# Kernel tuning notes

Hardware: AMD Instinct MI355X
Metric: run time of the kernel (lower is better)

Reference implementation:

```python
import jax, jax.numpy as jnp
import numpy as np

N_NODES = 100000
N_EDGES = 1600000
IN_FEATS = 128
HID = 128
N_GRAPHS = 1024


def setup_inputs() -> dict:
    key = jax.random.key(0)
    ks = jax.random.split(key, 10)
    h = jax.random.normal(ks[0], (N_NODES, IN_FEATS), dtype=jnp.float32)
    src = jax.random.randint(ks[1], (N_EDGES,), 0, N_NODES)
    dst = jax.random.randint(ks[2], (N_EDGES,), 0, N_NODES)
    graph_ids = jnp.sort(jax.random.randint(ks[3], (N_NODES,), 0, N_GRAPHS))
    # parameters (Glorot-ish scale)
    W1 = jax.random.normal(ks[4], (IN_FEATS, HID), dtype=jnp.float32) / np.sqrt(IN_FEATS)
    b1 = jnp.zeros((HID,), dtype=jnp.float32)
    W2 = jax.random.normal(ks[5], (HID, HID), dtype=jnp.float32) / np.sqrt(HID)
    b2 = jnp.zeros((HID,), dtype=jnp.float32)
    fc_w = jax.random.normal(ks[6], (HID, 1), dtype=jnp.float32) / np.sqrt(HID)
    fc_b = jnp.zeros((1,), dtype=jnp.float32)
    return {"h": h, "src": src, "dst": dst, "graph_ids": graph_ids,
            "n_graphs": N_GRAPHS, "W1": W1, "b1": b1, "W2": W2, "b2": b2,
            "fc_w": fc_w, "fc_b": fc_b}


def _graph_conv(x, W, b, src, dst, c_src, c_dst):
    # DGL GraphConv, norm='both': scale by out_deg^-1/2 at src, aggregate, scale by in_deg^-1/2 at dst
    x = (x * c_src) @ W                      # [N, out]
    agg = jax.ops.segment_sum(x[src], dst, num_segments=x.shape[0])  # SpMM via gather+scatter
    return agg * c_dst + b


def reference(h, src, dst, graph_ids, n_graphs, W1, b1, W2, b2, fc_w, fc_b):
    n = h.shape[0]
    ones_e = jnp.ones(src.shape[0], dtype=h.dtype)
    out_deg = jnp.clip(jax.ops.segment_sum(ones_e, src, num_segments=n), 1.0)
    in_deg = jnp.clip(jax.ops.segment_sum(ones_e, dst, num_segments=n), 1.0)
    c_src = (out_deg ** -0.5)[:, None]
    c_dst = (in_deg ** -0.5)[:, None]

    x = jax.nn.relu(_graph_conv(h, W1, b1, src, dst, c_src, c_dst))
    x = jax.nn.relu(_graph_conv(x, W2, b2, src, dst, c_src, c_dst))

    # dgl.mean_nodes: per-graph mean over nodes
    sums = jax.ops.segment_sum(x, graph_ids, num_segments=n_graphs)        # [G, HID]
    cnts = jnp.clip(jax.ops.segment_sum(jnp.ones((n,), x.dtype), graph_ids,
                                        num_segments=n_graphs), 1.0)
    hg = sums / cnts[:, None]
    return (hg @ fc_w + fc_b).squeeze(-1)    # [G]
```

## Files before the change

kernel.cpp:

```cpp
#include <hip/hip_runtime.h>


#define RANGE 256
#define NBMAX 1024
#define EPB 4096
#define CAP 5120

typedef __attribute__((ext_vector_type(4))) float facc4;
typedef __attribute__((ext_vector_type(8))) short bfrag8;

__device__ inline unsigned short f2bf(float x) {
  unsigned u = __float_as_uint(x);
  u += 0x7FFFu + ((u >> 16) & 1u);
  return (unsigned short)(u >> 16);
}
__device__ inline float bf2f(unsigned short b) {
  return __uint_as_float((unsigned)b << 16);
}
__device__ inline float bflo(unsigned u) { return __uint_as_float(u << 16); }
__device__ inline float bfhi(unsigned u) { return __uint_as_float(u & 0xFFFF0000u); }

__device__ inline void acc8(float* a, const uint4 v) {
  a[0] += bflo(v.x); a[1] += bfhi(v.x);
  a[2] += bflo(v.y); a[3] += bfhi(v.y);
  a[4] += bflo(v.z); a[5] += bfhi(v.z);
  a[6] += bflo(v.w); a[7] += bfhi(v.w);
}

__device__ inline void gather_node(const int* __restrict__ esrc,
                                   const unsigned short* __restrict__ Y,
                                   int beg, int end, int fo, float* acc) {
  int e = beg;
  for (; e < end && (e & 3); ++e) {
    const uint4 v = *(const uint4*)(Y + (size_t)esrc[e] * 128 + fo);
    acc8(acc, v);
  }
  for (; e + 8 <= end; e += 8) {
    const int4 s0 = *(const int4*)(esrc + e);
    const int4 s1 = *(const int4*)(esrc + e + 4);
    const uint4 v0 = *(const uint4*)(Y + (size_t)s0.x * 128 + fo);
    const uint4 v1 = *(const uint4*)(Y + (size_t)s0.y * 128 + fo);
    const uint4 v2 = *(const uint4*)(Y + (size_t)s0.z * 128 + fo);
    const uint4 v3 = *(const uint4*)(Y + (size_t)s0.w * 128 + fo);
    const uint4 v4 = *(const uint4*)(Y + (size_t)s1.x * 128 + fo);
    const uint4 v5 = *(const uint4*)(Y + (size_t)s1.y * 128 + fo);
    const uint4 v6 = *(const uint4*)(Y + (size_t)s1.z * 128 + fo);
    const uint4 v7 = *(const uint4*)(Y + (size_t)s1.w * 128 + fo);
    acc8(acc, v0); acc8(acc, v1); acc8(acc, v2); acc8(acc, v3);
    acc8(acc, v4); acc8(acc, v5); acc8(acc, v6); acc8(acc, v7);
  }
  if (e + 4 <= end) {
    const int4 s0 = *(const int4*)(esrc + e);
    const uint4 v0 = *(const uint4*)(Y + (size_t)s0.x * 128 + fo);
    const uint4 v1 = *(const uint4*)(Y + (size_t)s0.y * 128 + fo);
    const uint4 v2 = *(const uint4*)(Y + (size_t)s0.z * 128 + fo);
    const uint4 v3 = *(const uint4*)(Y + (size_t)s0.w * 128 + fo);
    acc8(acc, v0); acc8(acc, v1); acc8(acc, v2); acc8(acc, v3);
    e += 4;
  }
  for (; e < end; ++e) {
    const uint4 v = *(const uint4*)(Y + (size_t)esrc[e] * 128 + fo);
    acc8(acc, v);
  }
}

__global__ __launch_bounds__(256) void k_part(const int* __restrict__ src,
                                              const int* __restrict__ dst,
                                              int* __restrict__ curS,
                                              int* __restrict__ curD,
                                              unsigned char* __restrict__ outS,
                                              unsigned int* __restrict__ outD,
                                              int E, int NB) {
  __shared__ int sS[EPB];
  __shared__ int sD[EPB];
  __shared__ int hS[NBMAX];
  __shared__ int hD[NBMAX];
  const int t = threadIdx.x;
  for (int i = t; i < NB; i += 256) { hS[i] = 0; hD[i] = 0; }
  __syncthreads();
  const int e0 = blockIdx.x * EPB;
  #pragma unroll
  for (int i = 0; i < EPB / 256; ++i) {
    const int e = e0 + t + 256 * i;
    if (e < E) {
      const int sv = src[e], dv = dst[e];
      sS[t + 256 * i] = sv;
      sD[t + 256 * i] = dv;
      atomicAdd(&hS[sv >> 8], 1);
      atomicAdd(&hD[dv >> 8], 1);
    }
  }
  __syncthreads();
  for (int i = t; i < NB; i += 256) {
    int c = hS[i];
    hS[i] = c ? atomicAdd(&curS[i], c) : 0;
    c = hD[i];
    hD[i] = c ? atomicAdd(&curD[i], c) : 0;
  }
  __syncthreads();
  #pragma unroll
  for (int i = 0; i < EPB / 256; ++i) {
    const int e = e0 + t + 256 * i;
    if (e < E) {
      const int sv = sS[t + 256 * i], dv = sD[t + 256 * i];
      int p = atomicAdd(&hS[sv >> 8], 1);
      if (p < CAP) outS[(size_t)(sv >> 8) * CAP + p] = (unsigned char)(sv & 255);
      p = atomicAdd(&hD[dv >> 8], 1);
      if (p < CAP)
        outD[(size_t)(dv >> 8) * CAP + p] =
            ((unsigned)(dv & 255) << 24) | (unsigned)sv;
    }
  }
}

__global__ __launch_bounds__(256) void k_prep(
    const unsigned int* __restrict__ outD, const int* __restrict__ curD,
    int2* __restrict__ rng, int* __restrict__ esrc, float* __restrict__ cD,
    const unsigned char* __restrict__ outS, const int* __restrict__ curS,
    float* __restrict__ cS, const int* __restrict__ gid,
    int* __restrict__ gstart, float* __restrict__ gsum,
    int N, int NB, int G, int nbN) {
  __shared__ int hist[RANGE];
  __shared__ int scn[RANGE];
  const int b = blockIdx.x;
  const int t = threadIdx.x;

  if (b < NB) {
    const int beg = b * CAP;
    const int cnt = min(curD[b], CAP);
    hist[t] = 0;
    __syncthreads();
    for (int e = t; e < cnt; e += 256)
      atomicAdd(&hist[outD[beg + e] >> 24], 1);
    __syncthreads();
    const int deg = hist[t];
    scn[t] = deg;
    __syncthreads();
    #pragma unroll
    for (int o = 1; o < RANGE; o <<= 1) {
      int u = (t >= o) ? scn[t - o] : 0;
      __syncthreads();
      scn[t] += u;
      __syncthreads();
    }
    const int excl = scn[t] - deg;
    const int node = b * RANGE + t;
    if (node < N) {
      cD[node] = rsqrtf((float)(deg > 1 ? deg : 1));
      rng[node] = make_int2(beg + excl, beg + excl + deg);
    }
    scn[t] = excl;
    __syncthreads();
    for (int e = t; e < cnt; e += 256) {
      const unsigned w = outD[beg + e];
      const int pos = beg + atomicAdd(&scn[w >> 24], 1);
      esrc[pos] = (int)(w & 0x1FFFFu);
    }
  } else if (b < 2 * NB) {
    const int bb = b - NB;
    const int beg = bb * CAP;
    const int cnt = min(curS[bb], CAP);
    hist[t] = 0;
    __syncthreads();
    for (int e = t; e < cnt; e += 256)
      atomicAdd(&hist[outS[beg + e]], 1);
    __syncthreads();
    const int node = bb * RANGE + t;
    if (node < N) cS[node] = rsqrtf((float)(hist[t] > 1 ? hist[t] : 1));
  } else if (b < 2 * NB + nbN) {
    const int i = (b - 2 * NB) * 256 + t;
    if (i < N) {
      const int g = gid[i];
      if (i == 0) {
        for (int q = 0; q <= g; ++q) gstart[q] = 0;
      } else {
        const int gp = gid[i - 1];
        for (int q = gp + 1; q <= g; ++q) gstart[q] = i;
      }
      if (i == N - 1) {
        for (int q = g + 1; q <= G; ++q) gstart[q] = N;
      }
    }
  } else {
    const int i = (b - 2 * NB - nbN) * 256 + t;
    if (i < G) gsum[i] = 0.f;
  }
}

__global__ __launch_bounds__(256) void k_wprep2(const float* __restrict__ W1,
                                                const float* __restrict__ W2,
                                                unsigned short* __restrict__ Whi,
                                                unsigned short* __restrict__ Wlo) {
  const int g = blockIdx.x * 256 + threadIdx.x;
  const float* W = (g < 16384) ? W1 : W2;
  const int idx = g & 16383;
  const int i = idx & 7;
  const int l = (idx >> 3) & 63;
  const int nb = (idx >> 9) & 7;
  const int kc = idx >> 12;
  const int k = kc * 32 + ((l >> 4) << 3) + i;
  const int n = (nb << 4) + (l & 15);
  const float v = W[k * 128 + n];
  const unsigned short hi = f2bf(v);
  Whi[g] = hi;
  Wlo[g] = f2bf(v - bf2f(hi));
}

__global__ __launch_bounds__(256) void k_mgemm0(const float* __restrict__ Xf,
                                                const unsigned short* __restrict__ Whi,
                                                const unsigned short* __restrict__ Wlo,
                                                const float* __restrict__ cS,
                                                unsigned short* __restrict__ Y,
                                                int N) {
  const int t = threadIdx.x;
  const int wv = t >> 6;
  const int l = t & 63;
  const int lm = l & 15;
  const int lg = l >> 4;
  const int row0 = (blockIdx.x * 4 + wv) * 16;
  const int row = row0 + lm;
  const bool rv = row < N;
  const int rc = rv ? row : 0;
  const float csr = rv ? cS[rc] : 0.f;

  facc4 acc[8];
  #pragma unroll
  for (int nb = 0; nb < 8; ++nb) acc[nb] = (facc4){0.f, 0.f, 0.f, 0.f};

  #pragma unroll
  for (int kc = 0; kc < 4; ++kc) {
    const int k0 = kc * 32 + (lg << 3);
    const float4 x0 = *(const float4*)(Xf + (size_t)rc * 128 + k0);
    const float4 x1 = *(const float4*)(Xf + (size_t)rc * 128 + k0 + 4);
    float a[8] = {x0.x, x0.y, x0.z, x0.w, x1.x, x1.y, x1.z, x1.w};
    #pragma unroll
    for (int i = 0; i < 8; ++i) a[i] *= csr;
    bfrag8 ah, al;
    #pragma unroll
    for (int i = 0; i < 8; ++i) {
      const unsigned short hh = f2bf(a[i]);
      ah[i] = (short)hh;
      al[i] = (short)f2bf(a[i] - bf2f(hh));
    }
    const size_t kb = ((size_t)kc * 8) * 512 + (size_t)l * 8;
    #pragma unroll
    for (int nb = 0; nb < 8; ++nb) {
      const bfrag8 bh = *(const bfrag8*)(Whi + kb + (size_t)nb * 512);
      const bfrag8 bl = *(const bfrag8*)(Wlo + kb + (size_t)nb * 512);
      acc[nb] = __builtin_amdgcn_mfma_f32_16x16x32_bf16(ah, bh, acc[nb], 0, 0, 0);
      acc[nb] = __builtin_amdgcn_mfma_f32_16x16x32_bf16(ah, bl, acc[nb], 0, 0, 0);
      acc[nb] = __builtin_amdgcn_mfma_f32_16x16x32_bf16(al, bh, acc[nb], 0, 0, 0);
    }
  }

  #pragma unroll
  for (int j = 0; j < 4; ++j) {
    const int r = row0 + (lg << 2) + j;
    if (r < N) {
      #pragma unroll
      for (int nb = 0; nb < 8; ++nb)
        Y[(size_t)r * 128 + (nb << 4) + lm] = f2bf(acc[nb][j]);
    }
  }
}

__global__ __launch_bounds__(256) void k_gspmm(
    const int2* __restrict__ rng, const int* __restrict__ esrc,
    const unsigned short* __restrict__ Y1,
    const unsigned short* __restrict__ Whi,
    const unsigned short* __restrict__ Wlo,
    const float* __restrict__ cS, const float* __restrict__ cD,
    const float* __restrict__ bias, unsigned short* __restrict__ Y2, int N) {
  __shared__ float As[64][132];
  const int t = threadIdx.x;
  const int base = blockIdx.x * 64;

  {
    const int lane = t & 15;
    const int grp = t >> 4;
    const int fo = lane * 8;
    #pragma unroll
    for (int s = 0; s < 4; ++s) {
      const int nl = s * 16 + grp;
      const int node = base + nl;
      float acc[8] = {0.f, 0.f, 0.f, 0.f, 0.f, 0.f, 0.f, 0.f};
      if (node < N) {
        const int2 be = rng[node];
        gather_node(esrc, Y1, be.x, be.y, fo, acc);
      }
      *(float4*)&As[nl][fo] = make_float4(acc[0], acc[1], acc[2], acc[3]);
      *(float4*)&As[nl][fo + 4] = make_float4(acc[4], acc[5], acc[6], acc[7]);
    }
  }
  __syncthreads();

  const int wv = t >> 6;
  const int l = t & 63;
  const int lm = l & 15;
  const int lg = l >> 4;
  const int row0 = base + wv * 16;
  const int row = row0 + lm;
  const bool rv = row < N;
  const int rc = rv ? row : 0;
  const float csr = rv ? cS[rc] : 0.f;
  const float cdr = rv ? cD[rc] : 0.f;
  const int arow = wv * 16 + lm;

  facc4 acc[8];
  #pragma unroll
  for (int nb = 0; nb < 8; ++nb) acc[nb] = (facc4){0.f, 0.f, 0.f, 0.f};

  #pragma unroll
  for (int kc = 0; kc < 4; ++kc) {
    const int k0 = kc * 32 + (lg << 3);
    const float4 a0 = *(const float4*)&As[arow][k0];
    const float4 a1 = *(const float4*)&As[arow][k0 + 4];
    float a[8] = {a0.x, a0.y, a0.z, a0.w, a1.x, a1.y, a1.z, a1.w};
    const float4 b0 = *(const float4*)(bias + k0);
    const float4 b1v = *(const float4*)(bias + k0 + 4);
    const float bb[8] = {b0.x, b0.y, b0.z, b0.w, b1v.x, b1v.y, b1v.z, b1v.w};
    #pragma unroll
    for (int i = 0; i < 8; ++i)
      a[i] = fmaxf(fmaf(a[i], cdr, bb[i]), 0.f) * csr;
    bfrag8 ah, al;
    #pragma unroll
    for (int i = 0; i < 8; ++i) {
      const unsigned short hh = f2bf(a[i]);
      ah[i] = (short)hh;
      al[i] = (short)f2bf(a[i] - bf2f(hh));
    }
    const size_t kb = ((size_t)kc * 8) * 512 + (size_t)l * 8;
    #pragma unroll
    for (int nb = 0; nb < 8; ++nb) {
      const bfrag8 bh = *(const bfrag8*)(Whi + kb + (size_t)nb * 512);
      const bfrag8 bl = *(const bfrag8*)(Wlo + kb + (size_t)nb * 512);
      acc[nb] = __builtin_amdgcn_mfma_f32_16x16x32_bf16(ah, bh, acc[nb], 0, 0, 0);
      acc[nb] = __builtin_amdgcn_mfma_f32_16x16x32_bf16(ah, bl, acc[nb], 0, 0, 0);
      acc[nb] = __builtin_amdgcn_mfma_f32_16x16x32_bf16(al, bh, acc[nb], 0, 0, 0);
    }
  }

  #pragma unroll
  for (int j = 0; j < 4; ++j) {
    const int r = row0 + (lg << 2) + j;
    if (r < N) {
      #pragma unroll
      for (int nb = 0; nb < 8; ++nb)
        Y2[(size_t)r * 128 + (nb << 4) + lm] = f2bf(acc[nb][j]);
    }
  }
}

__global__ __launch_bounds__(256) void k_spmm1(const int2* __restrict__ rng,
                                               const int* __restrict__ esrc,
                                               const unsigned short* __restrict__ Y,
                                               const float* __restrict__ cD,
                                               const float* __restrict__ b2,
                                               const float* __restrict__ fcw,
                                               const int* __restrict__ gid,
                                               float* __restrict__ gsum, int N) {
  __shared__ float sVal[16];
  __shared__ int sGid[16];
  const int t = threadIdx.x;
  const int lane = t & 15;
  const int grp = t >> 4;
  const int node = blockIdx.x * 16 + grp;
  const int fo = lane * 8;

  float acc[8] = {0.f, 0.f, 0.f, 0.f, 0.f, 0.f, 0.f, 0.f};
  if (node < N) {
    const int2 be = rng[node];
    gather_node(esrc, Y, be.x, be.y, fo, acc);
  }

  float s = 0.f;
  if (node < N) {
    const float c = cD[node];
    const float4 bA = *(const float4*)(b2 + fo);
    const float4 bB = *(const float4*)(b2 + fo + 4);
    const float4 wA = *(const float4*)(fcw + fo);
    const float4 wB = *(const float4*)(fcw + fo + 4);
    s += fmaxf(fmaf(acc[0], c, bA.x), 0.f) * wA.x;
    s += fmaxf(fmaf(acc[1], c, bA.y), 0.f) * wA.y;
    s += fmaxf(fmaf(acc[2], c, bA.z), 0.f) * wA.z;
    s += fmaxf(fmaf(acc[3], c, bA.w), 0.f) * wA.w;
    s += fmaxf(fmaf(acc[4], c, bB.x), 0.f) * wB.x;
    s += fmaxf(fmaf(acc[5], c, bB.y), 0.f) * wB.y;
    s += fmaxf(fmaf(acc[6], c, bB.z), 0.f) * wB.z;
    s += fmaxf(fmaf(acc[7], c, bB.w), 0.f) * wB.w;
  }
  #pragma unroll
  for (int o = 8; o > 0; o >>= 1) s += __shfl_down(s, o, 16);
  if (lane == 0) {
    sVal[grp] = (node < N) ? s : 0.f;
    sGid[grp] = (node < N) ? gid[node] : -1;
  }
  __syncthreads();
  if (t == 0) {
    int cg = -1;
    float cs = 0.f;
    #pragma unroll
    for (int k = 0; k < 16; ++k) {
      const int g = sGid[k];
      if (g < 0) continue;
      if (g == cg) {
        cs += sVal[k];
      } else {
        if (cg >= 0) atomicAdd(&gsum[cg], cs);
        cg = g;
        cs = sVal[k];
      }
    }
    if (cg >= 0) atomicAdd(&gsum[cg], cs);
  }
}

__global__ __launch_bounds__(256) void k_final(const float* __restrict__ gsum,
                                               const int* __restrict__ gstart,
                                               const float* __restrict__ fcb,
                                               float* __restrict__ out, int G) {
  const int g = blockIdx.x * 256 + threadIdx.x;
  if (g < G) {
    const int cnt = gstart[g + 1] - gstart[g];
    out[g] = gsum[g] / fmaxf((float)cnt, 1.f) + fcb[0];
  }
}

extern "C" void kernel_launch(void* const* d_in, const int* in_sizes, int n_in,
                              void* d_out, int out_size, void* d_ws, size_t ws_size,
                              hipStream_t stream) {
  const float* h   = (const float*)d_in[0];
  const int*   src = (const int*)d_in[1];
  const int*   dst = (const int*)d_in[2];
  const int*   gid = (const int*)d_in[3];
  const float* W1  = (const float*)d_in[5];
  const float* b1  = (const float*)d_in[6];
  const float* W2  = (const float*)d_in[7];
  const float* b2  = (const float*)d_in[8];
  const float* fcw = (const float*)d_in[9];
  const float* fcb = (const float*)d_in[10];
  float* out = (float*)d_out;

  const int N = in_sizes[0] / 128;
  const int E = in_sizes[1];
  const int G = out_size;
  const int NB = (N + RANGE - 1) / RANGE;

  char* base = (char*)d_ws;
  size_t off = 0;
  auto alloc = [&](size_t bytes) -> void* {
    void* p = base + off;
    off += (bytes + 1023) & ~(size_t)1023;
    return p;
  };
  unsigned short* Y1 = (unsigned short*)alloc((size_t)N * 128 * 2);
  unsigned short* Y2 = (unsigned short*)alloc((size_t)N * 128 * 2);
  unsigned int*  outD = (unsigned int*)Y1;
  unsigned char* outS = (unsigned char*)Y1 + (size_t)NB * CAP * 4;
  float* cS     = (float*)alloc((size_t)N * 4);
  float* cD     = (float*)alloc((size_t)N * 4);
  int2*  rng    = (int2*)alloc((size_t)N * 8);
  int*   esrc   = (int*)alloc((size_t)NB * CAP * 4);
  int*   cur    = (int*)alloc((size_t)2 * NBMAX * 4);
  float* gsum   = (float*)alloc((size_t)G * 4);
  int*   gstart = (int*)alloc((size_t)(G + 1) * 4);
  unsigned short* Whi = (unsigned short*)alloc(32768 * 2);
  unsigned short* Wlo = (unsigned short*)alloc(32768 * 2);
  (void)ws_size; (void)n_in;

  hipMemsetAsync(cur, 0, (size_t)2 * NBMAX * 4, stream);

  const int nbP = (E + EPB - 1) / EPB;
  const int nbN = (N + 255) / 256;
  const int nbG = (G + 255) / 256;
  k_part<<<nbP, 256, 0, stream>>>(src, dst, cur, cur + NBMAX, outS, outD, E, NB);
  k_prep<<<2 * NB + nbN + nbG, 256, 0, stream>>>(outD, cur + NBMAX, rng, esrc,
                                                 cD, outS, cur, cS, gid, gstart,
                                                 gsum, N, NB, G, nbN);
  k_wprep2<<<128, 256, 0, stream>>>(W1, W2, Whi, Wlo);

  const int nbM = (N + 63) / 64;
  const int nbS = (N + 15) / 16;
  k_mgemm0<<<nbM, 256, 0, stream>>>(h, Whi, Wlo, cS, Y1, N);
  k_gspmm<<<nbM, 256, 0, stream>>>(rng, esrc, Y1, Whi + 16384, Wlo + 16384,
                                   cS, cD, b1, Y2, N);
  k_spmm1<<<nbS, 256, 0, stream>>>(rng, esrc, Y2, cD, b2, fcw, gid, gsum, N);
  k_final<<<nbG, 256, 0, stream>>>(gsum, gstart, fcb, out, G);
}
```

Before: 232.9 us.

## Shrink LDS in partition and gather-GEMM kernels, fold weight prep into prep

The partition kernel no longer stages src/dst in shared memory and instead re-reads them from global memory in the second pass, which frees 32KB of LDS per block. The gather+GEMM kernel now stores aggregated rows in LDS as bf16 with an XOR swizzle instead of padded fp32, halving its LDS footprint to allow more resident blocks. The weight bf16 split kernel is merged into k_prep as extra blocks, removing one launch. The costs are a second global read of the edge arrays and an extra bf16 rounding of the aggregated activations before the split-precision MFMA.

```diff
diff --git a/kernel.cpp b/kernel.cpp
--- a/kernel.cpp
+++ b/kernel.cpp
@@ -71,8 +71,6 @@
                                               unsigned char* __restrict__ outS,
                                               unsigned int* __restrict__ outD,
                                               int E, int NB) {
-  __shared__ int sS[EPB];
-  __shared__ int sD[EPB];
   __shared__ int hS[NBMAX];
   __shared__ int hD[NBMAX];
   const int t = threadIdx.x;
@@ -83,11 +81,8 @@
   for (int i = 0; i < EPB / 256; ++i) {
     const int e = e0 + t + 256 * i;
     if (e < E) {
-      const int sv = src[e], dv = dst[e];
-      sS[t + 256 * i] = sv;
-      sD[t + 256 * i] = dv;
-      atomicAdd(&hS[sv >> 8], 1);
-      atomicAdd(&hD[dv >> 8], 1);
+      atomicAdd(&hS[src[e] >> 8], 1);
+      atomicAdd(&hD[dst[e] >> 8], 1);
     }
   }
   __syncthreads();
@@ -102,7 +97,7 @@
   for (int i = 0; i < EPB / 256; ++i) {
     const int e = e0 + t + 256 * i;
     if (e < E) {
-      const int sv = sS[t + 256 * i], dv = sD[t + 256 * i];
+      const int sv = src[e], dv = dst[e];
       int p = atomicAdd(&hS[sv >> 8], 1);
       if (p < CAP) outS[(size_t)(sv >> 8) * CAP + p] = (unsigned char)(sv & 255);
       p = atomicAdd(&hD[dv >> 8], 1);
@@ -119,7 +114,9 @@
     const unsigned char* __restrict__ outS, const int* __restrict__ curS,
     float* __restrict__ cS, const int* __restrict__ gid,
     int* __restrict__ gstart, float* __restrict__ gsum,
-    int N, int NB, int G, int nbN) {
+    const float* __restrict__ W1, const float* __restrict__ W2,
+    unsigned short* __restrict__ Whi, unsigned short* __restrict__ Wlo,
+    int N, int NB, int G, int nbN, int nbG) {
   __shared__ int hist[RANGE];
   __shared__ int scn[RANGE];
   const int b = blockIdx.x;
@@ -181,29 +178,24 @@
         for (int q = g + 1; q <= G; ++q) gstart[q] = N;
       }
     }
-  } else {
+  } else if (b < 2 * NB + nbN + nbG) {
     const int i = (b - 2 * NB - nbN) * 256 + t;
     if (i < G) gsum[i] = 0.f;
-  }
-}
-
-__global__ __launch_bounds__(256) void k_wprep2(const float* __restrict__ W1,
-                                                const float* __restrict__ W2,
-                                                unsigned short* __restrict__ Whi,
-                                                unsigned short* __restrict__ Wlo) {
-  const int g = blockIdx.x * 256 + threadIdx.x;
-  const float* W = (g < 16384) ? W1 : W2;
-  const int idx = g & 16383;
-  const int i = idx & 7;
-  const int l = (idx >> 3) & 63;
-  const int nb = (idx >> 9) & 7;
-  const int kc = idx >> 12;
-  const int k = kc * 32 + ((l >> 4) << 3) + i;
-  const int n = (nb << 4) + (l & 15);
-  const float v = W[k * 128 + n];
-  const unsigned short hi = f2bf(v);
-  Whi[g] = hi;
-  Wlo[g] = f2bf(v - bf2f(hi));
+  } else {
+    const int g = (b - 2 * NB - nbN - nbG) * 256 + t;
+    const float* W = (g < 16384) ? W1 : W2;
+    const int idx = g & 16383;
+    const int i = idx & 7;
+    const int l = (idx >> 3) & 63;
+    const int nb = (idx >> 9) & 7;
+    const int kc = idx >> 12;
+    const int k = kc * 32 + ((l >> 4) << 3) + i;
+    const int n = (nb << 4) + (l & 15);
+    const float v = W[k * 128 + n];
+    const unsigned short hi = f2bf(v);
+    Whi[g] = hi;
+    Wlo[g] = f2bf(v - bf2f(hi));
+  }
 }
 
 __global__ __launch_bounds__(256) void k_mgemm0(const float* __restrict__ Xf,
@@ -271,7 +263,7 @@
     const unsigned short* __restrict__ Wlo,
     const float* __restrict__ cS, const float* __restrict__ cD,
     const float* __restrict__ bias, unsigned short* __restrict__ Y2, int N) {
-  __shared__ float As[64][132];
+  __shared__ unsigned short As[64 * 128];
   const int t = threadIdx.x;
   const int base = blockIdx.x * 64;
 
@@ -288,8 +280,12 @@
         const int2 be = rng[node];
         gather_node(esrc, Y1, be.x, be.y, fo, acc);
       }
-      *(float4*)&As[nl][fo] = make_float4(acc[0], acc[1], acc[2], acc[3]);
-      *(float4*)&As[nl][fo + 4] = make_float4(acc[4], acc[5], acc[6], acc[7]);
+      uint4 w;
+      w.x = (unsigned)f2bf(acc[0]) | ((unsigned)f2bf(acc[1]) << 16);
+      w.y = (unsigned)f2bf(acc[2]) | ((unsigned)f2bf(acc[3]) << 16);
+      w.z = (unsigned)f2bf(acc[4]) | ((unsigned)f2bf(acc[5]) << 16);
+      w.w = (unsigned)f2bf(acc[6]) | ((unsigned)f2bf(acc[7]) << 16);
+      *(uint4*)&As[nl * 128 + ((lane ^ (nl & 7)) << 3)] = w;
     }
   }
   __syncthreads();
@@ -313,9 +309,12 @@
   #pragma unroll
   for (int kc = 0; kc < 4; ++kc) {
     const int k0 = kc * 32 + (lg << 3);
-    const float4 a0 = *(const float4*)&As[arow][k0];
-    const float4 a1 = *(const float4*)&As[arow][k0 + 4];
-    float a[8] = {a0.x, a0.y, a0.z, a0.w, a1.x, a1.y, a1.z, a1.w};
+    const uint4 xb = *(const uint4*)&As[arow * 128 + (((k0 >> 3) ^ (arow & 7)) << 3)];
+    float a[8];
+    a[0] = bflo(xb.x); a[1] = bfhi(xb.x);
+    a[2] = bflo(xb.y); a[3] = bfhi(xb.y);
+    a[4] = bflo(xb.z); a[5] = bfhi(xb.z);
+    a[6] = bflo(xb.w); a[7] = bfhi(xb.w);
     const float4 b0 = *(const float4*)(bias + k0);
     const float4 b1v = *(const float4*)(bias + k0 + 4);
     const float bb[8] = {b0.x, b0.y, b0.z, b0.w, b1v.x, b1v.y, b1v.z, b1v.w};
@@ -474,10 +473,9 @@
   const int nbN = (N + 255) / 256;
   const int nbG = (G + 255) / 256;
   k_part<<<nbP, 256, 0, stream>>>(src, dst, cur, cur + NBMAX, outS, outD, E, NB);
-  k_prep<<<2 * NB + nbN + nbG, 256, 0, stream>>>(outD, cur + NBMAX, rng, esrc,
-                                                 cD, outS, cur, cS, gid, gstart,
-                                                 gsum, N, NB, G, nbN);
-  k_wprep2<<<128, 256, 0, stream>>>(W1, W2, Whi, Wlo);
+  k_prep<<<2 * NB + nbN + nbG + 128, 256, 0, stream>>>(
+      outD, cur + NBMAX, rng, esrc, cD, outS, cur, cS, gid, gstart, gsum,
+      W1, W2, Whi, Wlo, N, NB, G, nbN, nbG);
 
   const int nbM = (N + 63) / 64;
   const int nbS = (N + 15) / 16;
```

New measurement: 235.9 us. No clear change (+1.3%).
